# Optimization experiments

Hardware: AMD Instinct MI355X
Metric: run time of the kernel (lower is better)

The kernel has to match this reference:

```python
import jax, jax.numpy as jnp
import numpy as np


def setup_inputs() -> dict:
    key = jax.random.key(0)
    ks = jax.random.split(key, 8)
    N, T, D, H = 2048, 365, 16, 64
    s = lambda d: 1.0 / np.sqrt(d)
    return {
        "x": jax.random.normal(ks[0], (N, T, D), dtype=jnp.float32),
        "A": jax.random.uniform(ks[1], (N, N), dtype=jnp.float32) * (1.0 / N),
        "W_ih": jax.random.normal(ks[2], (D, 4 * H), dtype=jnp.float32) * s(D),
        "W_hh": jax.random.normal(ks[3], (H, 4 * H), dtype=jnp.float32) * s(H),
        "bias": jnp.zeros((4 * H,), dtype=jnp.float32),
        "W_q": jax.random.normal(ks[4], (H, H), dtype=jnp.float32) * s(H),
        "b_q": jnp.zeros((H,), dtype=jnp.float32),
        "W_dense": jax.random.normal(ks[5], (H, 1), dtype=jnp.float32) * s(H),
        "b_dense": jnp.zeros((1,), dtype=jnp.float32),
    }


def reference(x, A, W_ih, W_hh, bias, W_q, b_q, W_dense, b_dense):
    N, T, D = x.shape
    H = W_hh.shape[0]

    def step(carry, x_t):
        h, c = carry
        gates = x_t @ W_ih + h @ W_hh + bias  # [N, 4H]
        i_t = jax.nn.sigmoid(gates[:, :H])
        f_t = jax.nn.sigmoid(gates[:, H:2 * H])
        g_t = jnp.tanh(gates[:, 2 * H:3 * H])
        o_t = jax.nn.sigmoid(gates[:, 3 * H:])
        q_t = jnp.tanh(h @ W_q + b_q)          # [N, H]
        c = f_t * (c + A @ q_t) + i_t * g_t    # graph-conv injected into cell state
        h = o_t * jnp.tanh(c)
        return (h, c), h

    h0 = jnp.zeros((N, H), dtype=x.dtype)
    c0 = jnp.zeros((N, H), dtype=x.dtype)
    # scan over time: x -> [T, N, D]
    _, hs = jax.lax.scan(step, (h0, c0), jnp.swapaxes(x, 0, 1))
    hidden_seq = jnp.swapaxes(hs, 0, 1)        # [N, T, H]
    out = hidden_seq @ W_dense + b_dense       # [N, T, 1]
    return out
```

## Files before the change

### kernel.cpp

```cpp
#include <hip/hip_runtime.h>
#include <stdint.h>

#define NN 2048
#define TT 365
#define DD 16
#define HH 64
#define NBLK 128
#define NTHR 1024
#define SMEM_BYTES 150016
#define QSLOT_U32 65536

typedef __attribute__((ext_vector_type(8))) short bf16x8;
typedef __attribute__((ext_vector_type(4))) float f32x4;
typedef __attribute__((ext_vector_type(4))) unsigned int u32x4;

__device__ __forceinline__ unsigned short f2bf(float f) {
  union { float f; uint32_t u; } z; z.f = f;
  uint32_t r = z.u + 0x7fffu + ((z.u >> 16) & 1u);
  return (unsigned short)(r >> 16);
}
__device__ __forceinline__ float sigmoid_(float x) { return 1.f / (1.f + __expf(-x)); }
__device__ __forceinline__ float tanh_(float x) {
  float ax = fabsf(x);
  float e = __expf(-2.f * ax);
  float r = (1.f - e) / (1.f + e);
  return x < 0.f ? -r : r;
}
__device__ __forceinline__ bf16x8 asbf(u32x4 v) { return __builtin_bit_cast(bf16x8, v); }

__global__ __launch_bounds__(NTHR) __attribute__((amdgpu_waves_per_eu(4, 4)))
void rgcn_persist(
    const float* __restrict__ X, const float* __restrict__ Af,
    const float* __restrict__ Wih, const float* __restrict__ Whh,
    const float* __restrict__ Bias, const float* __restrict__ Wq,
    const float* __restrict__ Bq, const float* __restrict__ Wd,
    const float* __restrict__ Bd, float* __restrict__ Out,
    uint32_t* qRing, uint32_t* flags, int rdepth, int ringfull)
{
  extern __shared__ __align__(16) char smem[];
  unsigned short* afrag = (unsigned short*)smem;
  unsigned short* whxT  = (unsigned short*)(smem + 65536);
  unsigned short* wqT   = (unsigned short*)(smem + 118784);
  float*          sh_g  = (float*)(smem + 128000);
  f32x4*          sh_part = (f32x4*)(smem + 128000);
  unsigned short* sh_hx = (unsigned short*)(smem + 144640);
  unsigned int*   cnt   = (unsigned int*)(smem + 147968);

  const int tid = threadIdx.x;
  const int w = tid >> 6;
  const int c = tid & 63;
  const int base = blockIdx.x * 16;
  const int m = c & 15, quad = c >> 4;
  const int nt = w & 3, kh = w >> 2;

  for (int i = tid; i < 256 * 104; i += NTHR) {
    int n = i / 104, k = i - n * 104;
    float v = (k < 64) ? Whh[k * 256 + n] : (k < 80) ? Wih[(k - 64) * 256 + n] : 0.f;
    whxT[i] = f2bf(v);
  }
  for (int i = tid; i < 64 * 72; i += NTHR) {
    int n = i / 72, k = i - n * 72;
    wqT[i] = (k < 64) ? f2bf(Wq[k * 64 + n]) : (unsigned short)0;
  }
  for (int i = tid; i < 16 * NN; i += NTHR) {
    int r = i >> 11, k = i & (NN - 1);
    afrag[(k >> 5) * 512 + (((k >> 3) & 3) * 16 + r) * 8 + (k & 7)] =
        f2bf(Af[(size_t)(base + r) * NN + k]);
  }
  for (int i = tid; i < 16 * 104; i += NTHR) sh_hx[i] = 0;
  __syncthreads();
  if (c < 16) sh_hx[w * 104 + 64 + c] = f2bf(X[(size_t)(base + w) * (TT * DD) + c]);
  if (tid == 0) *cnt = 0u;
  __syncthreads();

  const float b_i = Bias[c], b_f = Bias[64 + c], b_g = Bias[128 + c], b_o = Bias[192 + c];
  const float wdc = Wd[c], bdc = Bd[0];
  const float bqv = (w < 4) ? Bq[w * 16 + m] : 0.f;
  const unsigned short* afp = afrag + (kh * 16) * 512 + c * 8;

  float creg = 0.f, hreg = 0.f;
  float o0 = 0.f, o1 = 0.f, o2 = 0.f, o3 = 0.f, o4 = 0.f, o5 = 0.f;
  float px = 0.f;

  const uint32_t qoff = (uint32_t)((kh * 32 + (quad >> 1)) * 2048 +
                                   (nt * 16 + m) * 32 + (quad & 1) * 16);
  const uint32_t poff = (uint32_t)(blockIdx.x * 2048 + (w * 16 + m) * 32 + quad * 8);

  if (w < 4) {
    unsigned short qb = f2bf(tanh_(bqv));
    uint32_t pp = (uint32_t)qb | ((uint32_t)qb << 16);
    unsigned long long v = (unsigned long long)pp | ((unsigned long long)pp << 32);
    unsigned long long* dst = (unsigned long long*)((char*)qRing + poff);
    __hip_atomic_store(dst, v, __ATOMIC_RELAXED, __HIP_MEMORY_SCOPE_AGENT);
    asm volatile("s_waitcnt vmcnt(0)" ::: "memory");
    if (c == 0) {
      unsigned old = atomicAdd(cnt, 1u);
      if (old == 3u)
        __hip_atomic_store(&flags[blockIdx.x * 16], 1u,
                           __ATOMIC_RELAXED, __HIP_MEMORY_SCOPE_AGENT);
    }
  }

  int slotR = 0;
  for (int t = 0; t < TT; ++t) {
    const int slotW = (slotR + 1 == rdepth) ? 0 : slotR + 1;

    if (((t & 1) == 0) && c < 32) {
      int tt = t + 1 + (c >> 4);
      px = (tt < TT) ? X[(size_t)(base + w) * (TT * DD) + tt * DD + (c & 15)] : 0.f;
    }

    f32x4 dg = {0.f, 0.f, 0.f, 0.f};
    {
      const unsigned short* ar = sh_hx + m * 104 + quad * 8;
      const unsigned short* br = whxT + (w * 16 + m) * 104 + quad * 8;
      #pragma unroll
      for (int ch = 0; ch < 3; ++ch)
        dg = __builtin_amdgcn_mfma_f32_16x16x32_bf16(*(const bf16x8*)(ar + ch * 32),
                                                     *(const bf16x8*)(br + ch * 32), dg, 0, 0, 0);
    }
    #pragma unroll
    for (int r = 0; r < 4; ++r)
      sh_g[(quad * 4 + r) * 260 + w * 16 + m] = dg[r];
    __syncthreads();

    float gi = sigmoid_(b_i + sh_g[w * 260 + c]);
    float gf = sigmoid_(b_f + sh_g[w * 260 + 64 + c]);
    float gg = tanh_  (b_g + sh_g[w * 260 + 128 + c]);
    float go = sigmoid_(b_o + sh_g[w * 260 + 192 + c]);

    if (w == 0) {
      const uint32_t target = (uint32_t)(t + 1);
      for (;;) {
        uint32_t f0 = __hip_atomic_load(&flags[c * 16],
                                        __ATOMIC_RELAXED, __HIP_MEMORY_SCOPE_AGENT);
        uint32_t f1 = __hip_atomic_load(&flags[(64 + c) * 16],
                                        __ATOMIC_RELAXED, __HIP_MEMORY_SCOPE_AGENT);
        if (__all((f0 >= target) && (f1 >= target))) break;
        __builtin_amdgcn_s_sleep(1);
      }
    }
    __syncthreads();
    if (!ringfull)
      __builtin_amdgcn_fence(__ATOMIC_ACQUIRE, "agent");

    const uint64_t qa =
        (uint64_t)((char*)qRing + (size_t)slotR * (QSLOT_U32 * 4) + qoff);
    u32x4 qv[16];
    #pragma unroll
    for (int ch = 0; ch < 16; ++ch)
      qv[ch] = *(const u32x4*)(qa + (uint64_t)(ch * 4096));

    f32x4 acc0 = {0.f,0.f,0.f,0.f}, acc1 = {0.f,0.f,0.f,0.f};
    #pragma unroll
    for (int ch = 0; ch < 16; ch += 2) {
      acc0 = __builtin_amdgcn_mfma_f32_16x16x32_bf16(
          *(const bf16x8*)(afp + ch * 512), asbf(qv[ch]), acc0, 0, 0, 0);
      acc1 = __builtin_amdgcn_mfma_f32_16x16x32_bf16(
          *(const bf16x8*)(afp + (ch + 1) * 512), asbf(qv[ch + 1]), acc1, 0, 0, 0);
    }
    sh_part[w * 65 + c] = acc0 + acc1;
    __syncthreads();

    f32x4 vs;
    {
      const f32x4* sp = sh_part;
      const int li = (w >> 2) * 16 + m;
      f32x4 p0 = sp[(0 * 4 + quad) * 65 + li];
      f32x4 p1 = sp[(1 * 4 + quad) * 65 + li];
      f32x4 p2 = sp[(2 * 4 + quad) * 65 + li];
      f32x4 p3 = sp[(3 * 4 + quad) * 65 + li];
      vs = (p0 + p1) + (p2 + p3);
    }
    float a01 = (w & 1) ? vs[1] : vs[0];
    float a23 = (w & 1) ? vs[3] : vs[2];
    float aqv = (w & 2) ? a23 : a01;

    creg = gf * (creg + aqv) + gi * gg;
    hreg = go * tanh_(creg);
    sh_hx[w * 104 + c] = f2bf(hreg);
    {
      float xw = (t & 1) ? __shfl(px, (c & 15) + 16) : px;
      if (c < 16) sh_hx[w * 104 + 64 + c] = f2bf(xw);
    }
    __syncthreads();

    if (w < 4 && t < TT - 1) {
      f32x4 dq = {0.f, 0.f, 0.f, 0.f};
      const unsigned short* ar = sh_hx + m * 104 + quad * 8;
      const unsigned short* br = wqT + (w * 16 + m) * 72 + quad * 8;
      #pragma unroll
      for (int k2 = 0; k2 < 2; ++k2)
        dq = __builtin_amdgcn_mfma_f32_16x16x32_bf16(*(const bf16x8*)(ar + k2 * 32),
                                                     *(const bf16x8*)(br + k2 * 32), dq, 0, 0, 0);
      unsigned short b0 = f2bf(tanh_(dq[0] + bqv));
      unsigned short b1 = f2bf(tanh_(dq[1] + bqv));
      unsigned short b2 = f2bf(tanh_(dq[2] + bqv));
      unsigned short b3 = f2bf(tanh_(dq[3] + bqv));
      unsigned long long v =
          (unsigned long long)((uint32_t)b0 | ((uint32_t)b1 << 16)) |
          ((unsigned long long)((uint32_t)b2 | ((uint32_t)b3 << 16)) << 32);
      unsigned long long* dst = (unsigned long long*)
          ((char*)qRing + (size_t)slotW * (QSLOT_U32 * 4) + poff);
      __hip_atomic_store(dst, v, __ATOMIC_RELAXED, __HIP_MEMORY_SCOPE_AGENT);
    }

    {
      float red = hreg * wdc;
      #pragma unroll
      for (int off = 32; off; off >>= 1) red += __shfl_xor(red, off);
      float ov = red + bdc;
      switch (t >> 6) {
        case 0: if (c == (t & 63)) o0 = ov; break;
        case 1: if (c == (t & 63)) o1 = ov; break;
        case 2: if (c == (t & 63)) o2 = ov; break;
        case 3: if (c == (t & 63)) o3 = ov; break;
        case 4: if (c == (t & 63)) o4 = ov; break;
        default: if (c == (t & 63)) o5 = ov; break;
      }
    }

    if (w < 4 && t < TT - 1) {
      asm volatile("s_waitcnt vmcnt(0)" ::: "memory");
      if (c == 0) {
        unsigned old = atomicAdd(cnt, 1u);
        if (old == (unsigned)(4 * t + 7))
          __hip_atomic_store(&flags[blockIdx.x * 16], (uint32_t)(t + 2),
                             __ATOMIC_RELAXED, __HIP_MEMORY_SCOPE_AGENT);
      }
    }

    slotR = slotW;
  }

  {
    float* orow = Out + (size_t)(base + w) * TT;
    orow[c] = o0;
    orow[64 + c] = o1;
    orow[128 + c] = o2;
    orow[192 + c] = o3;
    orow[256 + c] = o4;
    if (320 + c < TT) orow[320 + c] = o5;
  }
}

extern "C" void kernel_launch(void* const* d_in, const int* in_sizes, int n_in,
                              void* d_out, int out_size, void* d_ws, size_t ws_size,
                              hipStream_t stream) {
  const float* X    = (const float*)d_in[0];
  const float* Af   = (const float*)d_in[1];
  const float* Wih  = (const float*)d_in[2];
  const float* Whh  = (const float*)d_in[3];
  const float* Bias = (const float*)d_in[4];
  const float* Wq   = (const float*)d_in[5];
  const float* Bq   = (const float*)d_in[6];
  const float* Wd   = (const float*)d_in[7];
  const float* Bd   = (const float*)d_in[8];
  float* Out = (float*)d_out;

  char* ws = (char*)d_ws;
  uint32_t* flags = (uint32_t*)ws;
  uint32_t* qRing = (uint32_t*)(ws + 8192);

  long long avail = (long long)ws_size - 8192;
  int rdepth = (int)(avail / (QSLOT_U32 * 4));
  if (rdepth > TT + 1) rdepth = TT + 1;
  if (rdepth < 2) rdepth = 2;
  int ringfull = (rdepth >= TT + 1) ? 1 : 0;

  hipFuncSetAttribute((const void*)rgcn_persist,
                      hipFuncAttributeMaxDynamicSharedMemorySize, SMEM_BYTES);
  hipMemsetAsync(ws, 0, 8192, stream);
  hipLaunchKernelGGL(rgcn_persist, dim3(NBLK), dim3(NTHR), SMEM_BYTES, stream,
                     X, Af, Wih, Whh, Bias, Wq, Bq, Wd, Bd, Out, qRing, flags,
                     rdepth, ringfull);
}
```

Measured before the change: 2.026 ms.

## Distribute grid-flag polling across all waves and pipeline ring loads with MFMA

Each of the four producer waves now does its own global atomicAdd on the block flag, replacing the LDS counter whose last arriver stored the flag. Every wave polls the 32 source flags it needs itself, in place of wave 0 polling all 128 and releasing the block through a barrier. When the ring is fully resident, the q loads are issued as inline asm and the first half of the MFMAs starts after a partial vmcnt wait, overlapping load latency with compute. This aims to shorten the per-step cross-block synchronisation latency, at the cost of more global polling traffic and more atomics on the flags.

```diff
diff --git a/kernel.cpp b/kernel.cpp
--- a/kernel.cpp
+++ b/kernel.cpp
@@ -44,7 +44,6 @@
   float*          sh_g  = (float*)(smem + 128000);
   f32x4*          sh_part = (f32x4*)(smem + 128000);
   unsigned short* sh_hx = (unsigned short*)(smem + 144640);
-  unsigned int*   cnt   = (unsigned int*)(smem + 147968);
 
   const int tid = threadIdx.x;
   const int w = tid >> 6;
@@ -70,7 +69,6 @@
   for (int i = tid; i < 16 * 104; i += NTHR) sh_hx[i] = 0;
   __syncthreads();
   if (c < 16) sh_hx[w * 104 + 64 + c] = f2bf(X[(size_t)(base + w) * (TT * DD) + c]);
-  if (tid == 0) *cnt = 0u;
   __syncthreads();
 
   const float b_i = Bias[c], b_f = Bias[64 + c], b_g = Bias[128 + c], b_o = Bias[192 + c];
@@ -93,12 +91,7 @@
     unsigned long long* dst = (unsigned long long*)((char*)qRing + poff);
     __hip_atomic_store(dst, v, __ATOMIC_RELAXED, __HIP_MEMORY_SCOPE_AGENT);
     asm volatile("s_waitcnt vmcnt(0)" ::: "memory");
-    if (c == 0) {
-      unsigned old = atomicAdd(cnt, 1u);
-      if (old == 3u)
-        __hip_atomic_store(&flags[blockIdx.x * 16], 1u,
-                           __ATOMIC_RELAXED, __HIP_MEMORY_SCOPE_AGENT);
-    }
+    if (c == 0) atomicAdd(&flags[blockIdx.x * 16], 1u);
   }
 
   int slotR = 0;
@@ -128,36 +121,59 @@
     float gf = sigmoid_(b_f + sh_g[w * 260 + 64 + c]);
     float gg = tanh_  (b_g + sh_g[w * 260 + 128 + c]);
     float go = sigmoid_(b_o + sh_g[w * 260 + 192 + c]);
-
-    if (w == 0) {
-      const uint32_t target = (uint32_t)(t + 1);
+    __syncthreads();
+
+    {
+      const uint32_t target = 4u * (uint32_t)(t + 1);
+      const int src = 32 * kh + (c & 31);
       for (;;) {
-        uint32_t f0 = __hip_atomic_load(&flags[c * 16],
-                                        __ATOMIC_RELAXED, __HIP_MEMORY_SCOPE_AGENT);
-        uint32_t f1 = __hip_atomic_load(&flags[(64 + c) * 16],
-                                        __ATOMIC_RELAXED, __HIP_MEMORY_SCOPE_AGENT);
-        if (__all((f0 >= target) && (f1 >= target))) break;
+        uint32_t f = __hip_atomic_load(&flags[src * 16],
+                                       __ATOMIC_RELAXED, __HIP_MEMORY_SCOPE_AGENT);
+        if (__all((int)(f >= target))) break;
         __builtin_amdgcn_s_sleep(1);
       }
     }
-    __syncthreads();
     if (!ringfull)
       __builtin_amdgcn_fence(__ATOMIC_ACQUIRE, "agent");
 
     const uint64_t qa =
         (uint64_t)((char*)qRing + (size_t)slotR * (QSLOT_U32 * 4) + qoff);
     u32x4 qv[16];
-    #pragma unroll
-    for (int ch = 0; ch < 16; ++ch)
-      qv[ch] = *(const u32x4*)(qa + (uint64_t)(ch * 4096));
-
     f32x4 acc0 = {0.f,0.f,0.f,0.f}, acc1 = {0.f,0.f,0.f,0.f};
-    #pragma unroll
-    for (int ch = 0; ch < 16; ch += 2) {
-      acc0 = __builtin_amdgcn_mfma_f32_16x16x32_bf16(
-          *(const bf16x8*)(afp + ch * 512), asbf(qv[ch]), acc0, 0, 0, 0);
-      acc1 = __builtin_amdgcn_mfma_f32_16x16x32_bf16(
-          *(const bf16x8*)(afp + (ch + 1) * 512), asbf(qv[ch + 1]), acc1, 0, 0, 0);
+    if (ringfull) {
+      #pragma unroll
+      for (int ch = 0; ch < 16; ++ch)
+        asm volatile("global_load_dwordx4 %0, %1, off"
+                     : "=v"(qv[ch]) : "v"(qa + (uint64_t)(ch * 4096)) : "memory");
+      asm volatile("s_waitcnt vmcnt(8)" ::: "memory");
+      __builtin_amdgcn_sched_barrier(0);
+      #pragma unroll
+      for (int ch = 0; ch < 8; ch += 2) {
+        acc0 = __builtin_amdgcn_mfma_f32_16x16x32_bf16(
+            *(const bf16x8*)(afp + ch * 512), asbf(qv[ch]), acc0, 0, 0, 0);
+        acc1 = __builtin_amdgcn_mfma_f32_16x16x32_bf16(
+            *(const bf16x8*)(afp + (ch + 1) * 512), asbf(qv[ch + 1]), acc1, 0, 0, 0);
+      }
+      asm volatile("s_waitcnt vmcnt(0)" ::: "memory");
+      __builtin_amdgcn_sched_barrier(0);
+      #pragma unroll
+      for (int ch = 8; ch < 16; ch += 2) {
+        acc0 = __builtin_amdgcn_mfma_f32_16x16x32_bf16(
+            *(const bf16x8*)(afp + ch * 512), asbf(qv[ch]), acc0, 0, 0, 0);
+        acc1 = __builtin_amdgcn_mfma_f32_16x16x32_bf16(
+            *(const bf16x8*)(afp + (ch + 1) * 512), asbf(qv[ch + 1]), acc1, 0, 0, 0);
+      }
+    } else {
+      #pragma unroll
+      for (int ch = 0; ch < 16; ++ch)
+        qv[ch] = *(const u32x4*)(qa + (uint64_t)(ch * 4096));
+      #pragma unroll
+      for (int ch = 0; ch < 16; ch += 2) {
+        acc0 = __builtin_amdgcn_mfma_f32_16x16x32_bf16(
+            *(const bf16x8*)(afp + ch * 512), asbf(qv[ch]), acc0, 0, 0, 0);
+        acc1 = __builtin_amdgcn_mfma_f32_16x16x32_bf16(
+            *(const bf16x8*)(afp + (ch + 1) * 512), asbf(qv[ch + 1]), acc1, 0, 0, 0);
+      }
     }
     sh_part[w * 65 + c] = acc0 + acc1;
     __syncthreads();
@@ -222,12 +238,7 @@
 
     if (w < 4 && t < TT - 1) {
       asm volatile("s_waitcnt vmcnt(0)" ::: "memory");
-      if (c == 0) {
-        unsigned old = atomicAdd(cnt, 1u);
-        if (old == (unsigned)(4 * t + 7))
-          __hip_atomic_store(&flags[blockIdx.x * 16], (uint32_t)(t + 2),
-                             __ATOMIC_RELAXED, __HIP_MEMORY_SCOPE_AGENT);
-      }
+      if (c == 0) atomicAdd(&flags[blockIdx.x * 16], 1u);
     }
 
     slotR = slotW;
```

New measurement: 1.848 ms. -8.8%, faster.
